# Kernel tuning notes

Hardware: AMD Instinct MI355X
Metric: run time of the kernel (lower is better)

## Reference

```python
import jax, jax.numpy as jnp
import numpy as np

H = 16
DK = 64
NEG = -10000000000.0


def setup_inputs() -> dict:
    key = jax.random.key(0)
    ks = jax.random.split(key, 9)
    B, S, D = 4, 1024, 1024
    query = jax.random.normal(ks[0], (B, S, D), dtype=jnp.float32)
    k_in = jax.random.normal(ks[1], (B, S, D), dtype=jnp.float32)
    mask = jax.random.randint(ks[2], (B, S, S), 0, 2, dtype=jnp.int32)
    s = 1.0 / np.sqrt(DK)
    Wq = jax.random.uniform(ks[3], (DK, DK), jnp.float32, -s, s)
    bq = jax.random.uniform(ks[4], (DK,), jnp.float32, -s, s)
    Wk = jax.random.uniform(ks[5], (DK, DK), jnp.float32, -s, s)
    bk = jax.random.uniform(ks[6], (DK,), jnp.float32, -s, s)
    sh = 1.0 / np.sqrt(H)
    Wc = jax.random.uniform(ks[7], (1, H), jnp.float32, -sh, sh)
    bc = jax.random.uniform(ks[8], (1,), jnp.float32, -sh, sh)
    return {"query": query, "key": k_in, "mask": mask,
            "Wq": Wq, "bq": bq, "Wk": Wk, "bk": bk, "Wc": Wc, "bc": bc}


def reference(query, key, mask, Wq, bq, Wk, bk, Wc, bc):
    B = query.shape[0]
    # torch .view(B, h, -1, d_k): plain reshape (matches original exactly)
    q = query.reshape(B, H, -1, DK)
    k = key.reshape(B, H, -1, DK)
    q = jnp.tanh(jnp.einsum('bhsd,ed->bhse', q, Wq) + bq)   # per-head Linear + tanh
    k = jnp.tanh(jnp.einsum('bhsd,ed->bhse', k, Wk) + bk)
    scores = jnp.einsum('bhqd,bhkd->bhqk', q, k)            # [B,h,Sq,Sk]
    # score_comb Linear(h,1) applied over head axis, then squeeze
    comb = jnp.einsum('bhqk,h->bqk', scores, Wc[0]) + bc[0]  # [B,Sq,Sk]
    comb = jnp.where(mask == 0, NEG, comb)
    return jax.nn.softmax(comb, axis=-1)
```

## Files before the change

kernel.cpp:

```cpp
#include <hip/hip_runtime.h>
#include <hip/hip_bf16.h>

typedef __attribute__((ext_vector_type(8))) short short8;
typedef __attribute__((ext_vector_type(4))) float floatx4;
typedef __attribute__((ext_vector_type(4))) int intx4;

__device__ __forceinline__ unsigned short f2bf(float x) {
    union { float f; unsigned u; } v; v.f = x;
    unsigned r = v.u + 0x7fffu + ((v.u >> 16) & 1u);
    return (unsigned short)(r >> 16);
}

__device__ __forceinline__ short8 pack8(float4 a, float4 b) {
    short8 s;
    s[0] = (short)f2bf(a.x); s[1] = (short)f2bf(a.y);
    s[2] = (short)f2bf(a.z); s[3] = (short)f2bf(a.w);
    s[4] = (short)f2bf(b.x); s[5] = (short)f2bf(b.y);
    s[6] = (short)f2bf(b.z); s[7] = (short)f2bf(b.w);
    return s;
}

__device__ __forceinline__ float fast_tanh(float x) {
    float e = __expf(2.0f * x);
    return 1.0f - 2.0f * __builtin_amdgcn_rcpf(e + 1.0f);
}

__global__ __launch_bounds__(256) void proj_kernel(
    const float* __restrict__ qin, const float* __restrict__ kin,
    const float* __restrict__ Wq, const float* __restrict__ bq,
    const float* __restrict__ Wk, const float* __restrict__ bk,
    const float* __restrict__ Wc,
    unsigned short* __restrict__ qt, unsigned short* __restrict__ kt)
{
    __shared__ unsigned short scr[4][16 * 72];
    const int which = blockIdx.y;
    const float* in  = which ? kin : qin;
    const float* W   = which ? Wk  : Wq;
    const float* bi  = which ? bk  : bq;
    unsigned short* out = which ? kt : qt;

    const int tid  = threadIdx.x;
    const int lane = tid & 63;
    const int w    = tid >> 6;
    const int ln   = lane & 15;
    const int g    = lane >> 4;

    short8 wf[4][2];
    #pragma unroll
    for (int c = 0; c < 4; ++c)
        #pragma unroll
        for (int t = 0; t < 2; ++t) {
            const float* p = W + (c * 16 + ln) * 64 + t * 32 + (g << 3);
            wf[c][t] = pack8(*(const float4*)p, *(const float4*)(p + 4));
        }
    float be[4];
    #pragma unroll
    for (int c = 0; c < 4; ++c) be[c] = bi[c * 16 + ln];

    const int rb = blockIdx.x << 6;
    const int b  = rb >> 14;
    const int h  = (rb >> 10) & 15;
    const float sc = which ? 1.0f : Wc[h];

    const int r0 = rb + (w << 4);
    const int s0 = (rb & 1023) + (w << 4);
    floatx4 acc[4] = {{0,0,0,0},{0,0,0,0},{0,0,0,0},{0,0,0,0}};
    #pragma unroll
    for (int t = 0; t < 2; ++t) {
        const float* p = in + (r0 + ln) * 64 + t * 32 + (g << 3);
        short8 af = pack8(*(const float4*)p, *(const float4*)(p + 4));
        #pragma unroll
        for (int c = 0; c < 4; ++c)
            acc[c] = __builtin_amdgcn_mfma_f32_16x16x32_bf16(af, wf[c][t], acc[c], 0, 0, 0);
    }

    unsigned short* s_scr = scr[w];
    #pragma unroll
    for (int c = 0; c < 4; ++c)
        #pragma unroll
        for (int r = 0; r < 4; ++r)
            s_scr[((g << 2) + r) * 72 + (c << 4) + ln] =
                f2bf(fast_tanh(acc[c][r] + be[c]) * sc);
    __syncthreads();

    const int itg = (b << 6) + (s0 >> 4);
    unsigned short* obase = out + ((size_t)(itg * 32 + h * 2) << 9) + (lane << 3);
    #pragma unroll
    for (int e2 = 0; e2 < 2; ++e2) {
        short8 v = *(const short8*)&s_scr[ln * 72 + (e2 << 5) + (g << 3)];
        *(short8*)(obase + (e2 << 9)) = v;
    }
}

#define RVMAGIC 0x9E3779B97F4A7C15ULL

__global__ __launch_bounds__(1024, 4) void attn_kernel(
    const unsigned short* __restrict__ qt, const unsigned short* __restrict__ kt,
    const int* __restrict__ mask, float* __restrict__ out,
    float* __restrict__ psums, unsigned long long* __restrict__ pflags)
{
    __shared__ __align__(16) unsigned short Al[32768];
    __shared__ __align__(16) int Ml[32 * 516];
    __shared__ float red[16][32];
    __shared__ float tot0[32], tot1[32];

    const int tid  = threadIdx.x;
    const int lane = tid & 63;
    const int w    = tid >> 6;
    const int ln   = lane & 15;
    const int g    = lane >> 4;

    const int id  = blockIdx.x;
    const int b   = id & 3;
    const int qlo = (id >> 2) & 1;
    const int ks  = (id >> 3) & 1;
    const int qs  = ((id >> 4) << 1) | qlo;
    const int i0  = qs << 5;
    const int slot = (((b << 5) + qs) << 1) + ks;
    const int sib  = slot ^ 1;

    const unsigned short* aSrc = qt + ((size_t)((b << 6) + (qs << 1)) << 14);
    #pragma unroll
    for (int rr = 0; rr < 4; ++rr) {
        const int idx = (rr << 10) + tid;
        *(short8*)&Al[idx << 3] = *(const short8*)(aSrc + ((size_t)idx << 3));
    }
    const int* mSrc = mask + ((size_t)((b << 10) + i0) << 10) + (ks << 9);
    #pragma unroll
    for (int rr = 0; rr < 4; ++rr) {
        const int idx = (rr << 10) + tid;
        const int li  = idx >> 7;
        const int cj  = idx & 127;
        intx4 mv = __builtin_nontemporal_load((const intx4*)(mSrc + (li << 10) + (cj << 2)));
        *(intx4*)&Ml[li * 516 + (cj << 2)] = mv;
    }
    __syncthreads();

    const unsigned short* bP = kt + ((size_t)((b << 6) + (ks << 5) + (w << 1)) << 14) + (lane << 3);
    const unsigned short* a0 = &Al[lane << 3];
    const unsigned short* a1 = &Al[16384 + (lane << 3)];

    floatx4 acc[2][2] = {{{0,0,0,0},{0,0,0,0}},{{0,0,0,0},{0,0,0,0}}};

    short8 av0 = *(const short8*)a0;
    short8 av1 = *(const short8*)a1;
    short8 bv0 = *(const short8*)bP;
    short8 bv1 = *(const short8*)(bP + (1 << 14));

    for (int kc = 1; kc < 32; ++kc) {
        const int o = kc << 9;
        short8 an0 = *(const short8*)(a0 + o);
        short8 an1 = *(const short8*)(a1 + o);
        short8 bn0 = *(const short8*)(bP + o);
        short8 bn1 = *(const short8*)(bP + (1 << 14) + o);
        acc[0][0] = __builtin_amdgcn_mfma_f32_16x16x32_bf16(av0, bv0, acc[0][0], 0, 0, 0);
        acc[0][1] = __builtin_amdgcn_mfma_f32_16x16x32_bf16(av0, bv1, acc[0][1], 0, 0, 0);
        acc[1][0] = __builtin_amdgcn_mfma_f32_16x16x32_bf16(av1, bv0, acc[1][0], 0, 0, 0);
        acc[1][1] = __builtin_amdgcn_mfma_f32_16x16x32_bf16(av1, bv1, acc[1][1], 0, 0, 0);
        av0 = an0; av1 = an1; bv0 = bn0; bv1 = bn1;
    }
    acc[0][0] = __builtin_amdgcn_mfma_f32_16x16x32_bf16(av0, bv0, acc[0][0], 0, 0, 0);
    acc[0][1] = __builtin_amdgcn_mfma_f32_16x16x32_bf16(av0, bv1, acc[0][1], 0, 0, 0);
    acc[1][0] = __builtin_amdgcn_mfma_f32_16x16x32_bf16(av1, bv0, acc[1][0], 0, 0, 0);
    acc[1][1] = __builtin_amdgcn_mfma_f32_16x16x32_bf16(av1, bv1, acc[1][1], 0, 0, 0);

    float psum[2][4] = {{0.f,0.f,0.f,0.f},{0.f,0.f,0.f,0.f}};
    #pragma unroll
    for (int st = 0; st < 2; ++st)
        #pragma unroll
        for (int nt = 0; nt < 2; ++nt) {
            const int j = (w << 5) + (nt << 4) + ln;
            #pragma unroll
            for (int r = 0; r < 4; ++r) {
                const int mv = Ml[((st << 4) + (g << 2) + r) * 516 + j];
                float e = mv ? __expf(acc[st][nt][r]) : 0.0f;
                acc[st][nt][r] = e;
                psum[st][r] += e;
            }
        }
    #pragma unroll
    for (int off = 1; off < 16; off <<= 1)
        #pragma unroll
        for (int st = 0; st < 2; ++st)
            #pragma unroll
            for (int r = 0; r < 4; ++r) psum[st][r] += __shfl_xor(psum[st][r], off);
    if (ln == 0) {
        #pragma unroll
        for (int st = 0; st < 2; ++st)
            #pragma unroll
            for (int r = 0; r < 4; ++r)
                red[w][(st << 4) + (g << 2) + r] = psum[st][r];
    }
    __syncthreads();

    if (tid < 32) {
        float s = 0.f;
        #pragma unroll
        for (int ww = 0; ww < 16; ++ww) s += red[ww][tid];
        tot0[tid] = s;
        __hip_atomic_store(&psums[(slot << 5) + tid], s,
                           __ATOMIC_RELAXED, __HIP_MEMORY_SCOPE_AGENT);
    }
    __syncthreads();
    if (tid == 0) {
        __threadfence();
        __hip_atomic_store(&pflags[slot], RVMAGIC,
                           __ATOMIC_RELAXED, __HIP_MEMORY_SCOPE_AGENT);
        int guard = 0;
        while (__hip_atomic_load(&pflags[sib], __ATOMIC_RELAXED,
                                 __HIP_MEMORY_SCOPE_AGENT) != RVMAGIC) {
            __builtin_amdgcn_s_sleep(2);
            if (++guard > (1 << 22)) break;
        }
        __threadfence();
    }
    __syncthreads();
    if (tid < 32)
        tot1[tid] = __hip_atomic_load(&psums[(sib << 5) + tid],
                                      __ATOMIC_RELAXED, __HIP_MEMORY_SCOPE_AGENT);
    __syncthreads();

    float* ob = out + ((size_t)((b << 10) + i0) << 10) + (ks << 9);
    #pragma unroll
    for (int st = 0; st < 2; ++st) {
        #pragma unroll
        for (int r = 0; r < 4; ++r) {
            const int row = (st << 4) + (g << 2) + r;
            const float inv = 1.0f / (tot0[row] + tot1[row]);
            #pragma unroll
            for (int nt = 0; nt < 2; ++nt) {
                const int j = (w << 5) + (nt << 4) + ln;
                __builtin_nontemporal_store(acc[st][nt][r] * inv,
                                            &ob[((size_t)row << 10) + j]);
            }
        }
    }
}

extern "C" void kernel_launch(void* const* d_in, const int* in_sizes, int n_in,
                              void* d_out, int out_size, void* d_ws, size_t ws_size,
                              hipStream_t stream)
{
    const float* query = (const float*)d_in[0];
    const float* key   = (const float*)d_in[1];
    const int*   mask  = (const int*)d_in[2];
    const float* Wq    = (const float*)d_in[3];
    const float* bq    = (const float*)d_in[4];
    const float* Wk    = (const float*)d_in[5];
    const float* bk    = (const float*)d_in[6];
    const float* Wc    = (const float*)d_in[7];

    float* out = (float*)d_out;
    unsigned short* qt = (unsigned short*)d_ws;
    unsigned short* kt = qt + (size_t)4 * 1024 * 1024;
    char* extra = (char*)d_ws + (size_t)16 * 1024 * 1024;
    float* psums = (float*)extra;
    unsigned long long* pflags = (unsigned long long*)(extra + 32 * 1024);

    proj_kernel<<<dim3(1024, 2), 256, 0, stream>>>(query, key, Wq, bq, Wk, bk, Wc, qt, kt);
    attn_kernel<<<256, 1024, 0, stream>>>(qt, kt, mask, out, psums, pflags);
}
```

Measured before the change: 136.9 us.

## Halve attention block rows, widen per-wave key tile, prefetch mask and K early

```diff
diff --git a/kernel.cpp b/kernel.cpp
--- a/kernel.cpp
+++ b/kernel.cpp
@@ -67,7 +67,7 @@
     floatx4 acc[4] = {{0,0,0,0},{0,0,0,0},{0,0,0,0},{0,0,0,0}};
     #pragma unroll
     for (int t = 0; t < 2; ++t) {
-        const float* p = in + (r0 + ln) * 64 + t * 32 + (g << 3);
+        const float* p = in + (size_t)(r0 + ln) * 64 + t * 32 + (g << 3);
         short8 af = pack8(*(const float4*)p, *(const float4*)(p + 4));
         #pragma unroll
         for (int c = 0; c < 4; ++c)
@@ -94,15 +94,15 @@
 
 #define RVMAGIC 0x9E3779B97F4A7C15ULL
 
-__global__ __launch_bounds__(1024, 4) void attn_kernel(
+__global__ __launch_bounds__(512, 4) void attn_kernel(
     const unsigned short* __restrict__ qt, const unsigned short* __restrict__ kt,
     const int* __restrict__ mask, float* __restrict__ out,
     float* __restrict__ psums, unsigned long long* __restrict__ pflags)
 {
-    __shared__ __align__(16) unsigned short Al[32768];
-    __shared__ __align__(16) int Ml[32 * 516];
-    __shared__ float red[16][32];
-    __shared__ float tot0[32], tot1[32];
+    __shared__ __align__(16) unsigned short Al[16384];
+    __shared__ __align__(16) int Ml[16 * 516];
+    __shared__ float red[8][16];
+    __shared__ float tot0[16], tot1[16];
 
     const int tid  = threadIdx.x;
     const int lane = tid & 63;
@@ -115,90 +115,99 @@
     const int qlo = (id >> 2) & 1;
     const int ks  = (id >> 3) & 1;
     const int qs  = ((id >> 4) << 1) | qlo;
-    const int i0  = qs << 5;
-    const int slot = (((b << 5) + qs) << 1) + ks;
+    const int i0  = qs << 4;
+    const int slot = (((b << 6) + qs) << 1) + ks;
     const int sib  = slot ^ 1;
 
-    const unsigned short* aSrc = qt + ((size_t)((b << 6) + (qs << 1)) << 14);
+    const int* mSrc = mask + ((size_t)((b << 10) + i0) << 10) + (ks << 9);
+    intx4 mreg[4];
     #pragma unroll
     for (int rr = 0; rr < 4; ++rr) {
-        const int idx = (rr << 10) + tid;
+        const int idx = (rr << 9) + tid;
+        mreg[rr] = __builtin_nontemporal_load(
+            (const intx4*)(mSrc + ((idx >> 7) << 10) + ((idx & 127) << 2)));
+    }
+
+    const unsigned short* bP = kt + ((size_t)((b << 6) + (ks << 5) + (w << 2)) << 14) + (lane << 3);
+    short8 bv[2][4];
+    #pragma unroll
+    for (int p = 0; p < 2; ++p)
+        #pragma unroll
+        for (int nt = 0; nt < 4; ++nt)
+            bv[p][nt] = *(const short8*)(bP + (nt << 14) + (p << 9));
+
+    const unsigned short* aSrc = qt + ((size_t)((b << 6) + qs) << 14);
+    #pragma unroll
+    for (int rr = 0; rr < 4; ++rr) {
+        const int idx = (rr << 9) + tid;
         *(short8*)&Al[idx << 3] = *(const short8*)(aSrc + ((size_t)idx << 3));
     }
-    const int* mSrc = mask + ((size_t)((b << 10) + i0) << 10) + (ks << 9);
     #pragma unroll
     for (int rr = 0; rr < 4; ++rr) {
-        const int idx = (rr << 10) + tid;
-        const int li  = idx >> 7;
-        const int cj  = idx & 127;
-        intx4 mv = __builtin_nontemporal_load((const intx4*)(mSrc + (li << 10) + (cj << 2)));
-        *(intx4*)&Ml[li * 516 + (cj << 2)] = mv;
-    }
-    __syncthreads();
-
-    const unsigned short* bP = kt + ((size_t)((b << 6) + (ks << 5) + (w << 1)) << 14) + (lane << 3);
-    const unsigned short* a0 = &Al[lane << 3];
-    const unsigned short* a1 = &Al[16384 + (lane << 3)];
-
-    floatx4 acc[2][2] = {{{0,0,0,0},{0,0,0,0}},{{0,0,0,0},{0,0,0,0}}};
-
-    short8 av0 = *(const short8*)a0;
-    short8 av1 = *(const short8*)a1;
-    short8 bv0 = *(const short8*)bP;
-    short8 bv1 = *(const short8*)(bP + (1 << 14));
-
-    for (int kc = 1; kc < 32; ++kc) {
-        const int o = kc << 9;
-        short8 an0 = *(const short8*)(a0 + o);
-        short8 an1 = *(const short8*)(a1 + o);
-        short8 bn0 = *(const short8*)(bP + o);
-        short8 bn1 = *(const short8*)(bP + (1 << 14) + o);
-        acc[0][0] = __builtin_amdgcn_mfma_f32_16x16x32_bf16(av0, bv0, acc[0][0], 0, 0, 0);
-        acc[0][1] = __builtin_amdgcn_mfma_f32_16x16x32_bf16(av0, bv1, acc[0][1], 0, 0, 0);
-        acc[1][0] = __builtin_amdgcn_mfma_f32_16x16x32_bf16(av1, bv0, acc[1][0], 0, 0, 0);
-        acc[1][1] = __builtin_amdgcn_mfma_f32_16x16x32_bf16(av1, bv1, acc[1][1], 0, 0, 0);
-        av0 = an0; av1 = an1; bv0 = bn0; bv1 = bn1;
-    }
-    acc[0][0] = __builtin_amdgcn_mfma_f32_16x16x32_bf16(av0, bv0, acc[0][0], 0, 0, 0);
-    acc[0][1] = __builtin_amdgcn_mfma_f32_16x16x32_bf16(av0, bv1, acc[0][1], 0, 0, 0);
-    acc[1][0] = __builtin_amdgcn_mfma_f32_16x16x32_bf16(av1, bv0, acc[1][0], 0, 0, 0);
-    acc[1][1] = __builtin_amdgcn_mfma_f32_16x16x32_bf16(av1, bv1, acc[1][1], 0, 0, 0);
-
-    float psum[2][4] = {{0.f,0.f,0.f,0.f},{0.f,0.f,0.f,0.f}};
-    #pragma unroll
-    for (int st = 0; st < 2; ++st)
-        #pragma unroll
-        for (int nt = 0; nt < 2; ++nt) {
-            const int j = (w << 5) + (nt << 4) + ln;
-            #pragma unroll
-            for (int r = 0; r < 4; ++r) {
-                const int mv = Ml[((st << 4) + (g << 2) + r) * 516 + j];
-                float e = mv ? __expf(acc[st][nt][r]) : 0.0f;
-                acc[st][nt][r] = e;
-                psum[st][r] += e;
-            }
-        }
+        const int idx = (rr << 9) + tid;
+        *(intx4*)&Ml[(idx >> 7) * 516 + ((idx & 127) << 2)] = mreg[rr];
+    }
+    __syncthreads();
+
+    const unsigned short* aL = &Al[lane << 3];
+    short8 av[2];
+    av[0] = *(const short8*)(aL);
+    av[1] = *(const short8*)(aL + (1 << 9));
+
+    floatx4 acc[4] = {{0,0,0,0},{0,0,0,0},{0,0,0,0},{0,0,0,0}};
+
+    for (int kb = 0; kb < 30; kb += 2) {
+        #pragma unroll
+        for (int s = 0; s < 2; ++s) {
+            const int kc = kb + s;
+            acc[0] = __builtin_amdgcn_mfma_f32_16x16x32_bf16(av[s], bv[s][0], acc[0], 0, 0, 0);
+            acc[1] = __builtin_amdgcn_mfma_f32_16x16x32_bf16(av[s], bv[s][1], acc[1], 0, 0, 0);
+            acc[2] = __builtin_amdgcn_mfma_f32_16x16x32_bf16(av[s], bv[s][2], acc[2], 0, 0, 0);
+            acc[3] = __builtin_amdgcn_mfma_f32_16x16x32_bf16(av[s], bv[s][3], acc[3], 0, 0, 0);
+            const int o2 = (kc + 2) << 9;
+            bv[s][0] = *(const short8*)(bP + o2);
+            bv[s][1] = *(const short8*)(bP + (1 << 14) + o2);
+            bv[s][2] = *(const short8*)(bP + (2 << 14) + o2);
+            bv[s][3] = *(const short8*)(bP + (3 << 14) + o2);
+            av[s] = *(const short8*)(aL + o2);
+        }
+    }
+    #pragma unroll
+    for (int s = 0; s < 2; ++s) {
+        acc[0] = __builtin_amdgcn_mfma_f32_16x16x32_bf16(av[s], bv[s][0], acc[0], 0, 0, 0);
+        acc[1] = __builtin_amdgcn_mfma_f32_16x16x32_bf16(av[s], bv[s][1], acc[1], 0, 0, 0);
+        acc[2] = __builtin_amdgcn_mfma_f32_16x16x32_bf16(av[s], bv[s][2], acc[2], 0, 0, 0);
+        acc[3] = __builtin_amdgcn_mfma_f32_16x16x32_bf16(av[s], bv[s][3], acc[3], 0, 0, 0);
+    }
+
+    float psum[4] = {0.f, 0.f, 0.f, 0.f};
+    #pragma unroll
+    for (int nt = 0; nt < 4; ++nt) {
+        const int j = (w << 6) + (nt << 4) + ln;
+        #pragma unroll
+        for (int r = 0; r < 4; ++r) {
+            const int mv = Ml[((g << 2) + r) * 516 + j];
+            float e = mv ? __expf(acc[nt][r]) : 0.0f;
+            acc[nt][r] = e;
+            psum[r] += e;
+        }
+    }
     #pragma unroll
     for (int off = 1; off < 16; off <<= 1)
         #pragma unroll
-        for (int st = 0; st < 2; ++st)
-            #pragma unroll
-            for (int r = 0; r < 4; ++r) psum[st][r] += __shfl_xor(psum[st][r], off);
+        for (int r = 0; r < 4; ++r) psum[r] += __shfl_xor(psum[r], off);
     if (ln == 0) {
         #pragma unroll
-        for (int st = 0; st < 2; ++st)
-            #pragma unroll
-            for (int r = 0; r < 4; ++r)
-                red[w][(st << 4) + (g << 2) + r] = psum[st][r];
-    }
-    __syncthreads();
-
-    if (tid < 32) {
+        for (int r = 0; r < 4; ++r) red[w][(g << 2) + r] = psum[r];
+    }
+    __syncthreads();
+
+    if (tid < 16) {
         float s = 0.f;
         #pragma unroll
-        for (int ww = 0; ww < 16; ++ww) s += red[ww][tid];
+        for (int ww = 0; ww < 8; ++ww) s += red[ww][tid];
         tot0[tid] = s;
-        __hip_atomic_store(&psums[(slot << 5) + tid], s,
+        __hip_atomic_store(&psums[(slot << 4) + tid], s,
                            __ATOMIC_RELAXED, __HIP_MEMORY_SCOPE_AGENT);
     }
     __syncthreads();
@@ -215,24 +224,20 @@
         __threadfence();
     }
     __syncthreads();
-    if (tid < 32)
-        tot1[tid] = __hip_atomic_load(&psums[(sib << 5) + tid],
+    if (tid < 16)
+        tot1[tid] = __hip_atomic_load(&psums[(sib << 4) + tid],
                                       __ATOMIC_RELAXED, __HIP_MEMORY_SCOPE_AGENT);
     __syncthreads();
 
     float* ob = out + ((size_t)((b << 10) + i0) << 10) + (ks << 9);
     #pragma unroll
-    for (int st = 0; st < 2; ++st) {
-        #pragma unroll
-        for (int r = 0; r < 4; ++r) {
-            const int row = (st << 4) + (g << 2) + r;
-            const float inv = 1.0f / (tot0[row] + tot1[row]);
-            #pragma unroll
-            for (int nt = 0; nt < 2; ++nt) {
-                const int j = (w << 5) + (nt << 4) + ln;
-                __builtin_nontemporal_store(acc[st][nt][r] * inv,
-                                            &ob[((size_t)row << 10) + j]);
-            }
+    for (int r = 0; r < 4; ++r) {
+        const int row = (g << 2) + r;
+        const float inv = 1.0f / (tot0[row] + tot1[row]);
+        #pragma unroll
+        for (int nt = 0; nt < 4; ++nt) {
+            const int j = (w << 6) + (nt << 4) + ln;
+            ob[((size_t)row << 10) + j] = acc[nt][r] * inv;
         }
     }
 }
@@ -258,5 +263,5 @@
     unsigned long long* pflags = (unsigned long long*)(extra + 32 * 1024);
 
     proj_kernel<<<dim3(1024, 2), 256, 0, stream>>>(query, key, Wq, bq, Wk, bk, Wc, qt, kt);
-    attn_kernel<<<256, 1024, 0, stream>>>(qt, kt, mask, out, psums, pflags);
-}
+    attn_kernel<<<512, 512, 0, stream>>>(qt, kt, mask, out, psums, pflags);
+}
```

Measured after the change: 164.9 us. 1.2x slower.
